# Optimization experiments

Measured on AMD Instinct MI355X. Metric: run time of the kernel, lower is better.

Reference implementation:

```python
import jax, jax.numpy as jnp
import numpy as np
import math

B, S, D = 4, 2048, 1024
WINDOW = 10  # window_size; attends to |i-j| <= WINDOW//2


def setup_inputs() -> dict:
    key = jax.random.key(0)
    ks = jax.random.split(key, 9)
    sc = 1.0 / math.sqrt(D)
    return {
        "x": jax.random.normal(ks[0], (B, S, D), dtype=jnp.float32),
        "Wq": jax.random.normal(ks[1], (D, D), dtype=jnp.float32) * sc,
        "bq": jnp.zeros((D,), dtype=jnp.float32),
        "Wk": jax.random.normal(ks[2], (D, D), dtype=jnp.float32) * sc,
        "bk": jnp.zeros((D,), dtype=jnp.float32),
        "Wv": jax.random.normal(ks[3], (D, D), dtype=jnp.float32) * sc,
        "bv": jnp.zeros((D,), dtype=jnp.float32),
        "Wo": jax.random.normal(ks[4], (D, D), dtype=jnp.float32) * sc,
        "bo": jnp.zeros((D,), dtype=jnp.float32),
    }


def _local_mask(seq_len: int, window_size: int) -> jnp.ndarray:
    # row i attends to columns [i - w//2, i + w//2] inclusive -> |i - j| <= w//2
    i = jnp.arange(seq_len)[:, None]
    j = jnp.arange(seq_len)[None, :]
    return jnp.abs(i - j) <= (window_size // 2)  # [S, S] bool


def reference(x, Wq, bq, Wk, bk, Wv, bv, Wo, bo):
    # nn.Linear: y = x @ W.T + b
    Q = x @ Wq.T + bq  # [B, S, D]
    K = x @ Wk.T + bk
    V = x @ Wv.T + bv
    scores = jnp.einsum("bqd,bkd->bqk", Q, K) / jnp.float32(math.sqrt(D))
    mask = _local_mask(x.shape[1], WINDOW)
    scores = jnp.where(mask[None, :, :], scores, jnp.float32(-1e9))
    attn = jax.nn.softmax(scores, axis=-1)  # [B, S, S]
    context = jnp.einsum("bqk,bkd->bqd", attn, V)
    output = context @ Wo.T + bo
    return output, attn
```

## Files before the change

kernel.cpp:

```cpp
#include <hip/hip_runtime.h>
#include <hip/hip_bf16.h>
#include <cstdint>
#include <cstddef>


typedef __attribute__((ext_vector_type(8))) short bf16x8;
typedef __attribute__((ext_vector_type(4))) float f32x4;
typedef __attribute__((ext_vector_type(8))) unsigned short ushortx8;

#define GPTR(x) ((const __attribute__((address_space(1))) void*)(x))
#define LPTR(x) ((__attribute__((address_space(3))) void*)(x))

__device__ __forceinline__ unsigned short f2bf(float f) {
    __hip_bfloat16 h = __float2bfloat16(f);
    unsigned short u;
    __builtin_memcpy(&u, &h, 2);
    return u;
}
__device__ __forceinline__ float bf2f(unsigned short u) {
    unsigned int x = ((unsigned int)u) << 16;
    float f;
    __builtin_memcpy(&f, &x, 4);
    return f;
}

__global__ void prep1(const float* __restrict__ x,  const float* __restrict__ Wq,
                      const float* __restrict__ Wk, const float* __restrict__ Wv,
                      const float* __restrict__ Wo, const float* __restrict__ bv,
                      unsigned short* __restrict__ xh,
                      unsigned short* __restrict__ Woh,
                      unsigned short* __restrict__ Wqt,
                      unsigned short* __restrict__ Wkt,
                      unsigned short* __restrict__ Wvt,
                      float* __restrict__ bvo) {
    __shared__ float tl[64][65];
    const int bid = blockIdx.x;
    if (bid < 9216) {
        const int idx = bid * 256 + threadIdx.x;
        const float* src;
        unsigned short* dst;
        int off;
        if (idx < 2097152) { src = x;  dst = xh;  off = idx; }
        else               { src = Wo; dst = Woh; off = idx - 2097152; }
        f32x4 v = reinterpret_cast<const f32x4*>(src)[off];
        ushort4 o;
        o.x = f2bf(v[0]); o.y = f2bf(v[1]); o.z = f2bf(v[2]); o.w = f2bf(v[3]);
        reinterpret_cast<ushort4*>(dst)[off] = o;
    } else if (bid < 9984) {
        const int u   = bid - 9216;
        const int z   = u >> 8;
        const int rem = u & 255;
        const int by  = rem >> 4;
        const int bx  = rem & 15;
        const float* in = (z == 0) ? Wq : (z == 1) ? Wk : Wv;
        unsigned short* out = (z == 0) ? Wqt : (z == 1) ? Wkt : Wvt;
        const int t  = threadIdx.x;
        const int c  = t & 63;
        const int r4 = t >> 6;
#pragma unroll
        for (int i = 0; i < 16; ++i) {
            const int r = r4 * 16 + i;
            tl[r][c] = in[(size_t)(by * 64 + r) * 1024 + bx * 64 + c];
        }
        __syncthreads();
#pragma unroll
        for (int i = 0; i < 16; ++i) {
            const int r = r4 * 16 + i;
            out[(size_t)(bx * 64 + r) * 1024 + by * 64 + c] = f2bf(tl[c][r]);
        }
    } else {
        const int row  = (bid - 9984) * 4 + (threadIdx.x >> 6);
        const int lane = threadIdx.x & 63;
        float s = 0.f;
#pragma unroll
        for (int k = lane; k < 1024; k += 64)
            s += Wo[(size_t)row * 1024 + k] * bv[k];
#pragma unroll
        for (int off = 32; off >= 1; off >>= 1) s += __shfl_xor(s, off, 64);
        if (lane == 0) bvo[row] = s;
    }
}

__launch_bounds__(256, 4)
__global__ void gemv_w12(const unsigned short* __restrict__ Wqt,
                         const unsigned short* __restrict__ Wkt,
                         const float* __restrict__ bq, const float* __restrict__ bk,
                         float* __restrict__ w1, float* __restrict__ w2,
                         float* __restrict__ cbuf) {
    if (blockIdx.x == 256) {
        __shared__ float red[256];
        float pc = 0.f;
        for (int n = threadIdx.x; n < 1024; n += 256) pc += bq[n] * bk[n];
        red[threadIdx.x] = pc;
        __syncthreads();
        for (int s = 128; s > 0; s >>= 1) {
            if (threadIdx.x < s) red[threadIdx.x] += red[threadIdx.x + s];
            __syncthreads();
        }
        if (threadIdx.x == 0) cbuf[0] = red[0];
        return;
    }
    const int w    = threadIdx.x >> 6;
    const int lane = threadIdx.x & 63;
    const int d    = blockIdx.x * 4 + w;
    const int n0   = lane << 4;
    const unsigned short* krow = Wkt + (size_t)d * 1024 + n0;
    const unsigned short* qrow = Wqt + (size_t)d * 1024 + n0;
    ushortx8 ka = *reinterpret_cast<const ushortx8*>(krow);
    ushortx8 kb = *reinterpret_cast<const ushortx8*>(krow + 8);
    ushortx8 qa = *reinterpret_cast<const ushortx8*>(qrow);
    ushortx8 qb = *reinterpret_cast<const ushortx8*>(qrow + 8);
    float a1 = 0.f, a2 = 0.f;
#pragma unroll
    for (int t = 0; t < 8; ++t) {
        a1 += bq[n0 + t] * bf2f(ka[t]) + bq[n0 + 8 + t] * bf2f(kb[t]);
        a2 += bk[n0 + t] * bf2f(qa[t]) + bk[n0 + 8 + t] * bf2f(qb[t]);
    }
#pragma unroll
    for (int off = 32; off >= 1; off >>= 1) {
        a1 += __shfl_xor(a1, off, 64);
        a2 += __shfl_xor(a2, off, 64);
    }
    if (lane == 0) { w1[d] = a1; w2[d] = a2; }
}

__device__ __forceinline__ void gemm_core(const unsigned short* __restrict__ A,
                                          const unsigned short* __restrict__ Bw,
                                          int Kstride, int nk, int tm, int tn,
                                          unsigned short* As, unsigned short* Bs,
                                          f32x4 (&acc)[4][4]) {
    const int tid  = threadIdx.x;
    const int lane = tid & 63;
    const int w    = tid >> 6;
    const int wr   = w >> 1;
    const int wc   = w & 1;

    const int lrow8 = lane >> 3;
    const int lcolb = (lane & 7) << 4;

    const char* Abase = (const char*)(A + (size_t)tm * 128 * (size_t)Kstride);
    const char* Bbase = (const char*)(Bw + (size_t)tn * 128 * (size_t)Kstride);
    const size_t rstride = (size_t)Kstride * 2;

    for (int t = 0; t < nk; ++t) {
        const size_t k0b = ((size_t)t << 6) * 2;
#pragma unroll
        for (int ii = 0; ii < 4; ++ii) {
            const int c    = (w << 2) + ii;
            const int row  = (c << 3) + lrow8;
            const int csrc = lcolb ^ ((row & 7) << 4);
            __builtin_amdgcn_global_load_lds(
                GPTR(Abase + (size_t)row * rstride + k0b + (size_t)csrc),
                LPTR((char*)As + (c << 10)), 16, 0, 0);
            __builtin_amdgcn_global_load_lds(
                GPTR(Bbase + (size_t)row * rstride + k0b + (size_t)csrc),
                LPTR((char*)Bs + (c << 10)), 16, 0, 0);
        }
        __syncthreads();

#pragma unroll
        for (int kk = 0; kk < 2; ++kk) {
            bf16x8 af[4], bfr[4];
            const int cb = (kk << 6) + ((lane >> 4) << 4);
#pragma unroll
            for (int m = 0; m < 4; ++m) {
                const int row = (wr << 6) + (m << 4) + (lane & 15);
                af[m] = *reinterpret_cast<const bf16x8*>(
                    (const char*)As + row * 128 + (cb ^ ((row & 7) << 4)));
            }
#pragma unroll
            for (int n = 0; n < 4; ++n) {
                const int row = (wc << 6) + (n << 4) + (lane & 15);
                bfr[n] = *reinterpret_cast<const bf16x8*>(
                    (const char*)Bs + row * 128 + (cb ^ ((row & 7) << 4)));
            }
#pragma unroll
            for (int m = 0; m < 4; ++m)
#pragma unroll
                for (int n = 0; n < 4; ++n)
                    acc[m][n] = __builtin_amdgcn_mfma_f32_16x16x32_bf16(
                        af[m], bfr[n], acc[m][n], 0, 0, 0);
        }
        __syncthreads();
    }
}

__launch_bounds__(256, 3)
__global__ void splitk_r12(const unsigned short* __restrict__ Wqt,
                           const unsigned short* __restrict__ Wkt,
                           const unsigned short* __restrict__ Woh,
                           const unsigned short* __restrict__ Wvt,
                           float* __restrict__ part,
                           const unsigned short* __restrict__ xh,
                           const float* __restrict__ w1,
                           const float* __restrict__ w2,
                           const float* __restrict__ cbuf,
                           float* __restrict__ r1, float* __restrict__ r2) {
    __shared__ unsigned short As[128 * 64];
    __shared__ unsigned short Bs[128 * 64];
    const int bid = blockIdx.x;
    if (bid >= 512) {
        const int w    = threadIdx.x >> 6;
        const int lane = threadIdx.x & 63;
        const int g    = (bid - 512) * 4 + w;
        const unsigned short* row = xh + (size_t)g * 1024 + (lane << 4);
        ushortx8 xa = *reinterpret_cast<const ushortx8*>(row);
        ushortx8 xb = *reinterpret_cast<const ushortx8*>(row + 8);
        float a1 = 0.f, a2 = 0.f;
#pragma unroll
        for (int t = 0; t < 8; ++t) {
            const float xv = bf2f(xa[t]);
            const float xw = bf2f(xb[t]);
            a1 += xv * w1[(lane << 4) + t] + xw * w1[(lane << 4) + 8 + t];
            a2 += xv * w2[(lane << 4) + t] + xw * w2[(lane << 4) + 8 + t];
        }
#pragma unroll
        for (int off = 32; off >= 1; off >>= 1) {
            a1 += __shfl_xor(a1, off, 64);
            a2 += __shfl_xor(a2, off, 64);
        }
        if (lane == 0) { r1[g] = a1 + cbuf[0]; r2[g] = a2; }
        return;
    }

    f32x4 acc[4][4];
#pragma unroll
    for (int m = 0; m < 4; ++m)
#pragma unroll
        for (int n = 0; n < 4; ++n) acc[m][n] = (f32x4){0.f, 0.f, 0.f, 0.f};

    const int mat = bid >> 8;
    const int loc = bid & 255;
    const int ks  = loc >> 6;
    const int t64 = loc & 63;
    const int tm  = t64 >> 3;
    const int tn  = t64 & 7;

    const unsigned short* A = mat ? Woh : Wqt;
    const unsigned short* B = mat ? Wvt : Wkt;
    gemm_core(A + ks * 256, B + ks * 256, 1024, 4, tm, tn, As, Bs, acc);

    float* dst = part + ((size_t)(mat * 4 + ks) << 20);
    const int lane = threadIdx.x & 63;
    const int w    = threadIdx.x >> 6;
    const int wr   = w >> 1, wc = w & 1;
    const int col0 = (tn << 7) + (wc << 6) + (lane & 15);
    const int row0 = (tm << 7) + (wr << 6) + ((lane >> 4) << 2);
#pragma unroll
    for (int n = 0; n < 4; ++n) {
        const int col = col0 + (n << 4);
#pragma unroll
        for (int m = 0; m < 4; ++m) {
            const int row = row0 + (m << 4);
#pragma unroll
            for (int r = 0; r < 4; ++r)
                dst[(size_t)(row + r) * 1024 + col] = acc[m][n][r];
        }
    }
}

__global__ void reduce_wp(const float* __restrict__ part,
                          unsigned short* __restrict__ W2) {
    const int u = blockIdx.x * 256 + threadIdx.x;
    const int mat = u >> 18;
    const int off = u & 262143;
    const f32x4* p = reinterpret_cast<const f32x4*>(part);
    f32x4 s = p[((size_t)(mat * 4 + 0) << 18) + off];
    s += p[((size_t)(mat * 4 + 1) << 18) + off];
    s += p[((size_t)(mat * 4 + 2) << 18) + off];
    s += p[((size_t)(mat * 4 + 3) << 18) + off];
    ushort4 o;
    o.x = f2bf(s[0]); o.y = f2bf(s[1]); o.z = f2bf(s[2]); o.w = f2bf(s[3]);
    reinterpret_cast<ushort4*>(W2)[u] = o;
}

__launch_bounds__(256, 4)
__global__ void gemm_yv(const unsigned short* __restrict__ A,
                        const unsigned short* __restrict__ Bw,
                        const float* __restrict__ bvo,
                        unsigned short* __restrict__ C) {
    __shared__ unsigned short As[128 * 64];
    __shared__ unsigned short Bs[128 * 64];
    f32x4 acc[4][4];
#pragma unroll
    for (int m = 0; m < 4; ++m)
#pragma unroll
        for (int n = 0; n < 4; ++n) acc[m][n] = (f32x4){0.f, 0.f, 0.f, 0.f};

    const int sid = (blockIdx.x & 7) * (gridDim.x >> 3) + (blockIdx.x >> 3);
    const int tm  = sid >> 4;
    const int tn  = sid & 15;

    gemm_core(A, Bw, 1024, 16, tm, tn, As, Bs, acc);

    const int lane = threadIdx.x & 63;
    const int w    = threadIdx.x >> 6;
    const int wr   = w >> 1, wc = w & 1;
    const int seg  = tn >> 3;
    const int col0 = (tn << 7) + (wc << 6) + (lane & 15);
    const int row0 = (tm << 7) + (wr << 6) + ((lane >> 4) << 2);
#pragma unroll
    for (int n = 0; n < 4; ++n) {
        const int col = col0 + (n << 4);
        const float bb = seg ? bvo[col & 1023] : 0.f;
#pragma unroll
        for (int m = 0; m < 4; ++m) {
            const int row = row0 + (m << 4);
#pragma unroll
            for (int r = 0; r < 4; ++r)
                C[(size_t)(row + r) * 2048 + col] = f2bf(acc[m][n][r] + bb);
        }
    }
}

__launch_bounds__(256, 4)
__global__ void attn_band_kernel(const unsigned short* __restrict__ xh,
                                 const unsigned short* __restrict__ yVp,
                                 const float* __restrict__ r1,
                                 const float* __restrict__ r2,
                                 const float* __restrict__ bo,
                                 float* __restrict__ attn,
                                 float* __restrict__ outp) {
    __shared__ float psm[4][16];
    const int bid  = blockIdx.x;
    const int rb   = (bid & 7) * 256 + (bid >> 3);
    const int w    = threadIdx.x >> 6;
    const int lane = threadIdx.x & 63;
    const int g    = (rb << 2) + w;
    const int b    = g >> 11;
    const int i    = g & 2047;

    const unsigned short* qrow = xh + (size_t)g * 1024;
    float qf[16];
    {
        ushortx8 qa = *reinterpret_cast<const ushortx8*>(qrow + (lane << 4));
        ushortx8 qb = *reinterpret_cast<const ushortx8*>(qrow + (lane << 4) + 8);
#pragma unroll
        for (int t = 0; t < 8; ++t) { qf[t] = bf2f(qa[t]); qf[8 + t] = bf2f(qb[t]); }
    }
    const float r2g = r2[g];

    float s[11];
#pragma unroll
    for (int jj = 0; jj < 11; ++jj) {
        const int j = i - 5 + jj;
        const bool valid = ((unsigned)j < 2048u);
        const int jc = min(max(j, 0), 2047);
        const int gj = (b << 11) + jc;
        const unsigned short* krow = yVp + (size_t)gj * 2048;
        ushortx8 ka = *reinterpret_cast<const ushortx8*>(krow + (lane << 4));
        ushortx8 kb = *reinterpret_cast<const ushortx8*>(krow + (lane << 4) + 8);
        float d = 0.f;
#pragma unroll
        for (int t = 0; t < 8; ++t)
            d += qf[t] * bf2f(ka[t]) + qf[8 + t] * bf2f(kb[t]);
#pragma unroll
        for (int off = 32; off >= 1; off >>= 1) d += __shfl_xor(d, off, 64);
        s[jj] = valid ? (d + r2g + r1[gj]) * 0.03125f : -1e30f;
    }

    float mx = s[0];
#pragma unroll
    for (int jj = 1; jj < 11; ++jj) mx = fmaxf(mx, s[jj]);
    float p[11], sum = 0.f;
#pragma unroll
    for (int jj = 0; jj < 11; ++jj) { p[jj] = expf(s[jj] - mx); sum += p[jj]; }
    const float inv = 1.0f / sum;

    if (lane == 0) {
#pragma unroll
        for (int jj = 0; jj < 11; ++jj) psm[w][jj] = p[jj] * inv;
    }
    __syncthreads();

    const int lo = i - 5;
    float* arow = attn + (size_t)g * 2048;
#pragma unroll
    for (int e = 0; e < 8; ++e) {
        const int c0 = (e << 8) + (lane << 2);
        f32x4 v = (f32x4){0.f, 0.f, 0.f, 0.f};
        if (c0 + 3 >= lo && c0 <= lo + 10) {
#pragma unroll
            for (int t = 0; t < 4; ++t) {
                const int d = c0 + t - lo;
                if ((unsigned)d < 11u) v[t] = psm[w][d];
            }
        }
        *reinterpret_cast<f32x4*>(arow + c0) = v;
    }

    float cacc[16];
#pragma unroll
    for (int t = 0; t < 16; ++t) cacc[t] = 0.f;
#pragma unroll
    for (int jj = 0; jj < 11; ++jj) {
        const int j  = i - 5 + jj;
        const int jc = min(max(j, 0), 2047);
        const float pj = p[jj] * inv;
        const unsigned short* vrow = yVp + ((size_t)((b << 11) + jc)) * 2048 + 1024;
        ushortx8 va = *reinterpret_cast<const ushortx8*>(vrow + (lane << 4));
        ushortx8 vb = *reinterpret_cast<const ushortx8*>(vrow + (lane << 4) + 8);
#pragma unroll
        for (int t = 0; t < 8; ++t) {
            cacc[t]     += pj * bf2f(va[t]);
            cacc[8 + t] += pj * bf2f(vb[t]);
        }
    }
    const int c0 = lane << 4;
    float* op = outp + (size_t)g * 1024 + c0;
#pragma unroll
    for (int q = 0; q < 4; ++q) {
        f32x4 bb = *reinterpret_cast<const f32x4*>(bo + c0 + (q << 2));
        f32x4 o;
#pragma unroll
        for (int t = 0; t < 4; ++t) o[t] = cacc[(q << 2) + t] + bb[t];
        *reinterpret_cast<f32x4*>(op + (q << 2)) = o;
    }
}

extern "C" void kernel_launch(void* const* d_in, const int* in_sizes, int n_in,
                              void* d_out, int out_size, void* d_ws, size_t ws_size,
                              hipStream_t stream) {
    const float* x  = (const float*)d_in[0];
    const float* Wq = (const float*)d_in[1];
    const float* bq = (const float*)d_in[2];
    const float* Wk = (const float*)d_in[3];
    const float* bk = (const float*)d_in[4];
    const float* Wv = (const float*)d_in[5];
    const float* bv = (const float*)d_in[6];
    const float* Wo = (const float*)d_in[7];
    const float* bo = (const float*)d_in[8];

    const size_t MS = 8192, DD = 1024;

    float* out  = (float*)d_out;
    float* attn = out + MS * DD;

    char* ws = (char*)d_ws;
    unsigned short* xh   = (unsigned short*)ws; ws += MS * DD * 2;
    unsigned short* Woh  = (unsigned short*)ws; ws += DD * DD * 2;
    unsigned short* Wqt  = (unsigned short*)ws; ws += DD * DD * 2;
    unsigned short* Wkt  = (unsigned short*)ws; ws += DD * DD * 2;
    unsigned short* Wvt  = (unsigned short*)ws; ws += DD * DD * 2;
    float*          bvo  = (float*)ws;          ws += DD * 4;
    float*          w1   = (float*)ws;          ws += DD * 4;
    float*          w2   = (float*)ws;          ws += DD * 4;
    float*          cbuf = (float*)ws;          ws += 256;
    float*          r1   = (float*)ws;          ws += MS * 4;
    float*          r2   = (float*)ws;          ws += MS * 4;
    float*          part = (float*)ws;          ws += (size_t)8 * DD * DD * 4;
    unsigned short* W2   = (unsigned short*)ws; ws += 2 * DD * DD * 2;
    unsigned short* yVp  = (unsigned short*)ws; ws += MS * 2 * DD * 2;

    prep1<<<dim3(10240), dim3(256), 0, stream>>>(x, Wq, Wk, Wv, Wo, bv,
                                                 xh, Woh, Wqt, Wkt, Wvt, bvo);

    gemv_w12<<<dim3(257), dim3(256), 0, stream>>>(Wqt, Wkt, bq, bk, w1, w2, cbuf);

    splitk_r12<<<dim3(2560), dim3(256), 0, stream>>>(Wqt, Wkt, Woh, Wvt, part,
                                                     xh, w1, w2, cbuf, r1, r2);
    reduce_wp<<<dim3(2048), dim3(256), 0, stream>>>(part, W2);

    gemm_yv<<<dim3(1024), dim3(256), 0, stream>>>(xh, W2, bvo, yVp);

    attn_band_kernel<<<dim3(2048), dim3(256), 0, stream>>>(xh, yVp, r1, r2, bo,
                                                           attn, out);
}
```

Measured before the change: 121.6 us.

## Replace yV GEMM with 256x256-tile double-buffered LDS-direct-load kernel

Swaps the 128x128-tile gemm_yv for a 512-thread kernel that computes 256x256 output tiles. Each warp holds 8x4 MFMA accumulators, and A/B tiles are double-buffered in LDS through global_load_lds with an XOR swizzle, so the next K-tile's loads overlap compute. The bigger tiles cut global traffic per FLOP. In exchange the grid drops to 256 blocks at one block per CU, and it uses 128KB LDS and many accumulator registers, which may limit occupancy and latency hiding.

```diff
diff --git a/kernel.cpp b/kernel.cpp
--- a/kernel.cpp
+++ b/kernel.cpp
@@ -274,37 +274,124 @@
     reinterpret_cast<ushort4*>(W2)[u] = o;
 }
 
-__launch_bounds__(256, 4)
-__global__ void gemm_yv(const unsigned short* __restrict__ A,
-                        const unsigned short* __restrict__ Bw,
-                        const float* __restrict__ bvo,
-                        unsigned short* __restrict__ C) {
-    __shared__ unsigned short As[128 * 64];
-    __shared__ unsigned short Bs[128 * 64];
-    f32x4 acc[4][4];
-#pragma unroll
-    for (int m = 0; m < 4; ++m)
+__launch_bounds__(512, 1)
+__global__ void gemm_yv256(const unsigned short* __restrict__ A,
+                           const unsigned short* __restrict__ Bw,
+                           const float* __restrict__ bvo,
+                           unsigned short* __restrict__ C) {
+    __shared__ unsigned short As[2][2][128 * 64];
+    __shared__ unsigned short Bs[2][2][128 * 64];
+
+    const int tid  = threadIdx.x;
+    const int lane = tid & 63;
+    const int w    = tid >> 6;
+    const int wr   = w >> 2;
+    const int wc   = w & 3;
+    const int l15  = lane & 15;
+    const int cs   = lane >> 4;
+
+    const int chunk = gridDim.x >> 3;
+    const int sid   = (blockIdx.x & 7) * chunk + (blockIdx.x >> 3);
+    const int tm    = sid >> 3;
+    const int tn    = sid & 7;
+
+    const int p    = w >> 1;
+    const int isB  = p & 1;
+    const int half = p >> 1;
+    const unsigned short* G = isB ? Bw : A;
+    const int grow0 = (isB ? tn : tm) * 256 + half * 128;
+    const size_t rstride = 2048;
+    const int sbase = (w & 1) << 9;
+
+    int srow[8], scol[8];
+#pragma unroll
+    for (int q = 0; q < 8; ++q) {
+        const int slot = sbase + (q << 6) + lane;
+        srow[q] = slot >> 3;
+        scol[q] = ((slot & 7) << 4) ^ ((srow[q] & 7) << 4);
+    }
+
+    f32x4 acc[8][4];
+#pragma unroll
+    for (int m = 0; m < 8; ++m)
 #pragma unroll
         for (int n = 0; n < 4; ++n) acc[m][n] = (f32x4){0.f, 0.f, 0.f, 0.f};
 
-    const int sid = (blockIdx.x & 7) * (gridDim.x >> 3) + (blockIdx.x >> 3);
-    const int tm  = sid >> 4;
-    const int tn  = sid & 15;
-
-    gemm_core(A, Bw, 1024, 16, tm, tn, As, Bs, acc);
-
-    const int lane = threadIdx.x & 63;
-    const int w    = threadIdx.x >> 6;
-    const int wr   = w >> 1, wc = w & 1;
-    const int seg  = tn >> 3;
-    const int col0 = (tn << 7) + (wc << 6) + (lane & 15);
-    const int row0 = (tm << 7) + (wr << 6) + ((lane >> 4) << 2);
+    char* unitdst[2];
+    unitdst[0] = (isB ? (char*)Bs : (char*)As) + (half << 14);
+    unitdst[1] = unitdst[0] + (1 << 15);
+
+    {
+#pragma unroll
+        for (int q = 0; q < 8; ++q)
+            __builtin_amdgcn_global_load_lds(
+                GPTR((const char*)G + (size_t)(grow0 + srow[q]) * rstride + scol[q]),
+                LPTR(unitdst[0] + ((sbase + (q << 6)) << 4)), 16, 0, 0);
+    }
+
+    const char* Abase = (char*)As + (wr << 14);
+    const char* Bbase = (char*)Bs + ((wc >> 1) << 14);
+    const int   brow0 = (wc & 1) << 6;
+
+    const int NT = 16;
+    int buf = 0;
+    for (int t = 0; t < NT; ++t) {
+        __builtin_amdgcn_s_barrier();
+        if (t + 1 < NT) {
+            const size_t kb = (size_t)(t + 1) << 7;
+            char* dst = unitdst[buf ^ 1];
+#pragma unroll
+            for (int q = 0; q < 8; ++q)
+                __builtin_amdgcn_global_load_lds(
+                    GPTR((const char*)G + (size_t)(grow0 + srow[q]) * rstride + kb + scol[q]),
+                    LPTR(dst + ((sbase + (q << 6)) << 4)), 16, 0, 0);
+            asm volatile("s_waitcnt vmcnt(8)" ::: "memory");
+        } else {
+            asm volatile("s_waitcnt vmcnt(0)" ::: "memory");
+        }
+        __builtin_amdgcn_s_barrier();
+
+        const char* Ab = Abase + (buf << 15);
+        const char* Bb = Bbase + (buf << 15);
+#pragma unroll
+        for (int kk = 0; kk < 2; ++kk) {
+            bf16x8 bfr[4];
+#pragma unroll
+            for (int n = 0; n < 4; ++n) {
+                const int row = brow0 + (n << 4) + l15;
+                bfr[n] = *reinterpret_cast<const bf16x8*>(
+                    Bb + row * 128 + (((kk << 6) + (cs << 4)) ^ ((row & 7) << 4)));
+            }
+#pragma unroll
+            for (int mh = 0; mh < 2; ++mh) {
+                bf16x8 af[4];
+#pragma unroll
+                for (int m = 0; m < 4; ++m) {
+                    const int row = (mh << 6) + (m << 4) + l15;
+                    af[m] = *reinterpret_cast<const bf16x8*>(
+                        Ab + row * 128 + (((kk << 6) + (cs << 4)) ^ ((row & 7) << 4)));
+                }
+                __builtin_amdgcn_s_setprio(1);
+#pragma unroll
+                for (int m = 0; m < 4; ++m)
+#pragma unroll
+                    for (int n = 0; n < 4; ++n)
+                        acc[mh * 4 + m][n] = __builtin_amdgcn_mfma_f32_16x16x32_bf16(
+                            af[m], bfr[n], acc[mh * 4 + m][n], 0, 0, 0);
+                __builtin_amdgcn_s_setprio(0);
+            }
+        }
+        buf ^= 1;
+    }
+
+    const int col0 = tn * 256 + wc * 64 + l15;
+    const int row0 = tm * 256 + wr * 128 + (cs << 2);
 #pragma unroll
     for (int n = 0; n < 4; ++n) {
         const int col = col0 + (n << 4);
-        const float bb = seg ? bvo[col & 1023] : 0.f;
-#pragma unroll
-        for (int m = 0; m < 4; ++m) {
+        const float bb = (col >= 1024) ? bvo[col & 1023] : 0.f;
+#pragma unroll
+        for (int m = 0; m < 8; ++m) {
             const int row = row0 + (m << 4);
 #pragma unroll
             for (int r = 0; r < 4; ++r)
@@ -461,7 +548,7 @@
                                                      xh, w1, w2, cbuf, r1, r2);
     reduce_wp<<<dim3(2048), dim3(256), 0, stream>>>(part, W2);
 
-    gemm_yv<<<dim3(1024), dim3(256), 0, stream>>>(xh, W2, bvo, yVp);
+    gemm_yv256<<<dim3(256), dim3(512), 0, stream>>>(xh, W2, bvo, yVp);
 
     attn_band_kernel<<<dim3(2048), dim3(256), 0, stream>>>(xh, yVp, r1, r2, bo,
                                                            attn, out);
```

After: 122.8 us. No clear change (+1.0%).

## Fuse bias GEMV into prep kernel and split-K reduction into GEMM via atomic counter

Applied to the files above, without the earlier changes.

The separate gemv_w12 kernel is removed. The bias-weight products are now computed from the fp32 weights inside the prep kernel as 8 partial chunks, and the r1/r2 blocks sum those partials themselves. The reduce_wp kernel is also removed: each split-K GEMM tile bumps an atomic counter, and the last of the four blocks to finish sums the partials and writes the bf16 result. This cuts two kernel launches and their pipeline bubbles, at the cost of threadfence/atomic synchronisation and a serialized reduction tail in the last block of each tile.

```diff
diff --git a/kernel.cpp b/kernel.cpp
--- a/kernel.cpp
+++ b/kernel.cpp
@@ -24,15 +24,19 @@
     return f;
 }
 
-__global__ void prep1(const float* __restrict__ x,  const float* __restrict__ Wq,
+__global__ void prep2(const float* __restrict__ x,  const float* __restrict__ Wq,
                       const float* __restrict__ Wk, const float* __restrict__ Wv,
                       const float* __restrict__ Wo, const float* __restrict__ bv,
+                      const float* __restrict__ bq, const float* __restrict__ bk,
                       unsigned short* __restrict__ xh,
                       unsigned short* __restrict__ Woh,
                       unsigned short* __restrict__ Wqt,
                       unsigned short* __restrict__ Wkt,
                       unsigned short* __restrict__ Wvt,
-                      float* __restrict__ bvo) {
+                      float* __restrict__ bvo,
+                      float* __restrict__ wpart,
+                      float* __restrict__ cbuf,
+                      int* __restrict__ cnt) {
     __shared__ float tl[64][65];
     const int bid = blockIdx.x;
     if (bid < 9216) {
@@ -68,7 +72,7 @@
             const int r = r4 * 16 + i;
             out[(size_t)(bx * 64 + r) * 1024 + by * 64 + c] = f2bf(tl[c][r]);
         }
-    } else {
+    } else if (bid < 10240) {
         const int row  = (bid - 9984) * 4 + (threadIdx.x >> 6);
         const int lane = threadIdx.x & 63;
         float s = 0.f;
@@ -78,16 +82,22 @@
 #pragma unroll
         for (int off = 32; off >= 1; off >>= 1) s += __shfl_xor(s, off, 64);
         if (lane == 0) bvo[row] = s;
-    }
-}
-
-__launch_bounds__(256, 4)
-__global__ void gemv_w12(const unsigned short* __restrict__ Wqt,
-                         const unsigned short* __restrict__ Wkt,
-                         const float* __restrict__ bq, const float* __restrict__ bk,
-                         float* __restrict__ w1, float* __restrict__ w2,
-                         float* __restrict__ cbuf) {
-    if (blockIdx.x == 256) {
+    } else if (bid < 10304) {
+        const int u     = bid - 10240;
+        const int mat   = u >> 5;
+        const int rest  = u & 31;
+        const int chunk = rest >> 2;
+        const int dg    = rest & 3;
+        const int d     = dg * 256 + threadIdx.x;
+        const float* W  = mat ? Wq : Wk;
+        const float* bs = mat ? bk : bq;
+        float acc = 0.f;
+        const int n0 = chunk * 128;
+        for (int n = n0; n < n0 + 128; ++n)
+            acc += bs[n] * W[(size_t)n * 1024 + d];
+        wpart[(size_t)(mat * 8 + chunk) * 1024 + d] = acc;
+    } else {
+        if (threadIdx.x < 128) cnt[threadIdx.x] = 0;
         __shared__ float red[256];
         float pc = 0.f;
         for (int n = threadIdx.x; n < 1024; n += 256) pc += bq[n] * bk[n];
@@ -98,30 +108,7 @@
             __syncthreads();
         }
         if (threadIdx.x == 0) cbuf[0] = red[0];
-        return;
-    }
-    const int w    = threadIdx.x >> 6;
-    const int lane = threadIdx.x & 63;
-    const int d    = blockIdx.x * 4 + w;
-    const int n0   = lane << 4;
-    const unsigned short* krow = Wkt + (size_t)d * 1024 + n0;
-    const unsigned short* qrow = Wqt + (size_t)d * 1024 + n0;
-    ushortx8 ka = *reinterpret_cast<const ushortx8*>(krow);
-    ushortx8 kb = *reinterpret_cast<const ushortx8*>(krow + 8);
-    ushortx8 qa = *reinterpret_cast<const ushortx8*>(qrow);
-    ushortx8 qb = *reinterpret_cast<const ushortx8*>(qrow + 8);
-    float a1 = 0.f, a2 = 0.f;
-#pragma unroll
-    for (int t = 0; t < 8; ++t) {
-        a1 += bq[n0 + t] * bf2f(ka[t]) + bq[n0 + 8 + t] * bf2f(kb[t]);
-        a2 += bk[n0 + t] * bf2f(qa[t]) + bk[n0 + 8 + t] * bf2f(qb[t]);
-    }
-#pragma unroll
-    for (int off = 32; off >= 1; off >>= 1) {
-        a1 += __shfl_xor(a1, off, 64);
-        a2 += __shfl_xor(a2, off, 64);
-    }
-    if (lane == 0) { w1[d] = a1; w2[d] = a2; }
+    }
 }
 
 __device__ __forceinline__ void gemm_core(const unsigned short* __restrict__ A,
@@ -191,9 +178,10 @@
                            const unsigned short* __restrict__ Woh,
                            const unsigned short* __restrict__ Wvt,
                            float* __restrict__ part,
+                           unsigned short* __restrict__ W2,
+                           int* __restrict__ cnt,
                            const unsigned short* __restrict__ xh,
-                           const float* __restrict__ w1,
-                           const float* __restrict__ w2,
+                           const float* __restrict__ wpart,
                            const float* __restrict__ cbuf,
                            float* __restrict__ r1, float* __restrict__ r2) {
     __shared__ unsigned short As[128 * 64];
@@ -203,6 +191,20 @@
         const int w    = threadIdx.x >> 6;
         const int lane = threadIdx.x & 63;
         const int g    = (bid - 512) * 4 + w;
+        const f32x4* wp4 = reinterpret_cast<const f32x4*>(wpart);
+        f32x4 w1x[4], w2x[4];
+#pragma unroll
+        for (int q = 0; q < 4; ++q) {
+            w1x[q] = (f32x4){0.f, 0.f, 0.f, 0.f};
+            w2x[q] = (f32x4){0.f, 0.f, 0.f, 0.f};
+        }
+#pragma unroll
+        for (int c = 0; c < 8; ++c)
+#pragma unroll
+            for (int q = 0; q < 4; ++q) {
+                w1x[q] += wp4[(c << 8) + (lane << 2) + q];
+                w2x[q] += wp4[2048 + (c << 8) + (lane << 2) + q];
+            }
         const unsigned short* row = xh + (size_t)g * 1024 + (lane << 4);
         ushortx8 xa = *reinterpret_cast<const ushortx8*>(row);
         ushortx8 xb = *reinterpret_cast<const ushortx8*>(row + 8);
@@ -211,8 +213,8 @@
         for (int t = 0; t < 8; ++t) {
             const float xv = bf2f(xa[t]);
             const float xw = bf2f(xb[t]);
-            a1 += xv * w1[(lane << 4) + t] + xw * w1[(lane << 4) + 8 + t];
-            a2 += xv * w2[(lane << 4) + t] + xw * w2[(lane << 4) + 8 + t];
+            a1 += xv * w1x[t >> 2][t & 3] + xw * w1x[2 + (t >> 2)][t & 3];
+            a2 += xv * w2x[t >> 2][t & 3] + xw * w2x[2 + (t >> 2)][t & 3];
         }
 #pragma unroll
         for (int off = 32; off >= 1; off >>= 1) {
@@ -257,21 +259,30 @@
                 dst[(size_t)(row + r) * 1024 + col] = acc[m][n][r];
         }
     }
-}
-
-__global__ void reduce_wp(const float* __restrict__ part,
-                          unsigned short* __restrict__ W2) {
-    const int u = blockIdx.x * 256 + threadIdx.x;
-    const int mat = u >> 18;
-    const int off = u & 262143;
-    const f32x4* p = reinterpret_cast<const f32x4*>(part);
-    f32x4 s = p[((size_t)(mat * 4 + 0) << 18) + off];
-    s += p[((size_t)(mat * 4 + 1) << 18) + off];
-    s += p[((size_t)(mat * 4 + 2) << 18) + off];
-    s += p[((size_t)(mat * 4 + 3) << 18) + off];
-    ushort4 o;
-    o.x = f2bf(s[0]); o.y = f2bf(s[1]); o.z = f2bf(s[2]); o.w = f2bf(s[3]);
-    reinterpret_cast<ushort4*>(W2)[u] = o;
+
+    __shared__ int lastFlag;
+    __threadfence();
+    __syncthreads();
+    if (threadIdx.x == 0)
+        lastFlag = (atomicAdd(&cnt[mat * 64 + t64], 1) == 3);
+    __syncthreads();
+    if (lastFlag) {
+        __threadfence();
+        const size_t pbase = (size_t)(mat * 4) << 20;
+        for (int u = threadIdx.x; u < 4096; u += 256) {
+            const int rl = u >> 5;
+            const int cu = u & 31;
+            const size_t eoff = (size_t)(tm * 128 + rl) * 1024 + tn * 128 + cu * 4;
+            f32x4 s = *reinterpret_cast<const f32x4*>(part + pbase + eoff);
+            s += *reinterpret_cast<const f32x4*>(part + pbase + (1u << 20) + eoff);
+            s += *reinterpret_cast<const f32x4*>(part + pbase + (2u << 20) + eoff);
+            s += *reinterpret_cast<const f32x4*>(part + pbase + (3u << 20) + eoff);
+            ushort4 o;
+            o.x = f2bf(s[0]); o.y = f2bf(s[1]); o.z = f2bf(s[2]); o.w = f2bf(s[3]);
+            *reinterpret_cast<ushort4*>(
+                W2 + (size_t)(mat * 1024 + tm * 128 + rl) * 1024 + tn * 128 + cu * 4) = o;
+        }
+    }
 }
 
 __launch_bounds__(256, 4)
@@ -443,23 +454,22 @@
     unsigned short* Wkt  = (unsigned short*)ws; ws += DD * DD * 2;
     unsigned short* Wvt  = (unsigned short*)ws; ws += DD * DD * 2;
     float*          bvo  = (float*)ws;          ws += DD * 4;
-    float*          w1   = (float*)ws;          ws += DD * 4;
-    float*          w2   = (float*)ws;          ws += DD * 4;
+    float*          wpart= (float*)ws;          ws += 16 * DD * 4;
     float*          cbuf = (float*)ws;          ws += 256;
+    int*            cnt  = (int*)ws;            ws += 512;
     float*          r1   = (float*)ws;          ws += MS * 4;
     float*          r2   = (float*)ws;          ws += MS * 4;
     float*          part = (float*)ws;          ws += (size_t)8 * DD * DD * 4;
     unsigned short* W2   = (unsigned short*)ws; ws += 2 * DD * DD * 2;
     unsigned short* yVp  = (unsigned short*)ws; ws += MS * 2 * DD * 2;
 
-    prep1<<<dim3(10240), dim3(256), 0, stream>>>(x, Wq, Wk, Wv, Wo, bv,
-                                                 xh, Woh, Wqt, Wkt, Wvt, bvo);
-
-    gemv_w12<<<dim3(257), dim3(256), 0, stream>>>(Wqt, Wkt, bq, bk, w1, w2, cbuf);
+    prep2<<<dim3(10305), dim3(256), 0, stream>>>(x, Wq, Wk, Wv, Wo, bv, bq, bk,
+                                                 xh, Woh, Wqt, Wkt, Wvt, bvo,
+                                                 wpart, cbuf, cnt);
 
     splitk_r12<<<dim3(2560), dim3(256), 0, stream>>>(Wqt, Wkt, Woh, Wvt, part,
-                                                     xh, w1, w2, cbuf, r1, r2);
-    reduce_wp<<<dim3(2048), dim3(256), 0, stream>>>(part, W2);
+                                                     W2, cnt, xh, wpart, cbuf,
+                                                     r1, r2);
 
     gemm_yv<<<dim3(1024), dim3(256), 0, stream>>>(xh, W2, bvo, yVp);
 
```

After: 219.7 us. +80.7%, slower.
